# Optimization experiments

Measured on AMD Instinct MI355X. Metric: run time of the kernel, lower is better.

The kernel has to match this reference:

```python
import jax, jax.numpy as jnp
import numpy as np

QMIN, QMAX = -128, 127  # int8 range


def _quantize(x, scale, zero_point):
    """Affine quantize float -> int8: clamp(round(x/scale) + zp, -128, 127)."""
    q = jnp.round(x / scale) + zero_point
    return jnp.clip(q, QMIN, QMAX).astype(jnp.int8)


def setup_inputs() -> dict:
    key = jax.random.key(0)
    k1, k2, k3 = jax.random.split(key, 3)
    N, IN, OUT = 8192, 4096, 4096
    inp = jax.random.normal(k1, (N, IN), dtype=jnp.float32)
    # int8 weight table [OUT, IN]
    weight = jax.random.randint(k2, (OUT, IN), QMIN, QMAX + 1, dtype=jnp.int32).astype(jnp.int8)
    # int32 bias [OUT]
    bias = jax.random.randint(k3, (OUT,), -(2 ** 15), 2 ** 15, dtype=jnp.int32)
    return {
        "input": inp,
        "weight": weight,
        "bias": bias,
        "input_scale": 0.02,
        "input_zero_point": 0,
        "output_scale": 4096.0,
        "output_zero_point": 0,
    }


def reference(input, weight, bias, input_scale, input_zero_point, output_scale, output_zero_point):
    # 1) affine quantize input to int8
    q_input = _quantize(input, input_scale, input_zero_point)
    # 2) int32 matmul: F.linear(q_input.int32, weight.int32, bias.int32)
    acc = jnp.matmul(q_input.astype(jnp.int32), weight.astype(jnp.int32).T) + bias  # [N, OUT] int32
    # 3) requantize int32 accumulator to int8 with output scale/zero-point
    q_output = _quantize(acc.astype(jnp.float32), output_scale, output_zero_point)
    return q_output
```

## Files before the change

kernel.cpp:

```cpp
#include <hip/hip_runtime.h>
#include <stdint.h>

typedef int v4i __attribute__((ext_vector_type(4)));
typedef int v16i __attribute__((ext_vector_type(16)));

__device__ __forceinline__ int clamp_i8(int v) {
    return v < -128 ? -128 : (v > 127 ? 127 : v);
}

__device__ __forceinline__ void async_load16(const void* g, void* l) {
    __builtin_amdgcn_global_load_lds(
        (const __attribute__((address_space(1))) void*)g,
        (__attribute__((address_space(3))) void*)l, 16, 0, 0);
}

__global__ void quant_input_kernel(const float4* __restrict__ x, int* __restrict__ q,
                                   const float* __restrict__ scale_p,
                                   const int* __restrict__ zp_p, int n4) {
    const float inv = 1.0f / *scale_p;
    const int zp = *zp_p;
    const int stride = gridDim.x * blockDim.x;
    for (int t = blockIdx.x * blockDim.x + threadIdx.x; t < n4; t += stride) {
        float4 v = x[t];
        int q0 = clamp_i8((int)rintf(v.x * inv) + zp);
        int q1 = clamp_i8((int)rintf(v.y * inv) + zp);
        int q2 = clamp_i8((int)rintf(v.z * inv) + zp);
        int q3 = clamp_i8((int)rintf(v.w * inv) + zp);
        q[t] = (q0 & 255) | ((q1 & 255) << 8) | ((q2 & 255) << 16) | ((q3 & 255) << 24);
    }
}

__global__ void pack_weight_kernel(const int4* __restrict__ w, int* __restrict__ q, int n4) {
    const int stride = gridDim.x * blockDim.x;
    for (int t = blockIdx.x * blockDim.x + threadIdx.x; t < n4; t += stride) {
        int4 v = w[t];
        q[t] = (v.x & 255) | ((v.y & 255) << 8) | ((v.z & 255) << 16) | ((v.w & 255) << 24);
    }
}

#define BM 256
#define BN 128
#define BK 64

__global__ __launch_bounds__(256, 2) void gemm_i8_kernel(
    const int8_t* __restrict__ A, const int8_t* __restrict__ W,
    const int* __restrict__ bias, int* __restrict__ C,
    const float* __restrict__ oscale_p, const int* __restrict__ ozp_p,
    int N, int K, int M) {
    __shared__ int8_t lA[2][BM * BK];
    __shared__ int8_t lB[2][BN * BK];

    const int tid = threadIdx.x;
    const int lane = tid & 63;
    const int w = tid >> 6;
    const int wm = w >> 1;
    const int wn = w & 1;

    const int bm = blockIdx.y * BM;
    const int bn = blockIdx.x * BN;

    const int s_sub = lane >> 2;
    const int s_col = (((lane & 3) ^ ((s_sub >> 1) & 3))) * 16;
    const int8_t* gA = A + (int64_t)(bm + w * 64 + s_sub) * K + s_col;
    const int8_t* gB = W + (int64_t)(bn + w * 32 + s_sub) * K + s_col;
    const int64_t rs = (int64_t)16 * K;
    int8_t* lA0 = &lA[0][w * 4096];
    int8_t* lA1 = &lA[1][w * 4096];
    int8_t* lB0 = &lB[0][w * 2048];
    int8_t* lB1 = &lB[1][w * 2048];

    const int m0 = lane & 31;
    const int rsw = (m0 >> 1) & 3;
    const int chi = lane >> 5;

    v16i acc[4][2];
#pragma unroll
    for (int i = 0; i < 4; i++)
#pragma unroll
        for (int j = 0; j < 2; j++)
#pragma unroll
            for (int r = 0; r < 16; r++) acc[i][j][r] = 0;

    {
        async_load16(gA, lA0);
        async_load16(gA + rs, lA0 + 1024);
        async_load16(gA + 2 * rs, lA0 + 2048);
        async_load16(gA + 3 * rs, lA0 + 3072);
        async_load16(gB, lB0);
        async_load16(gB + rs, lB0 + 1024);
        gA += BK;
        gB += BK;
    }

    int cur = 0;
    for (int kt = 0; kt < K; kt += BK) {
        __syncthreads();
        if (kt + BK < K) {
            int8_t* dA = cur ? lA0 : lA1;
            int8_t* dB = cur ? lB0 : lB1;
            async_load16(gA, dA);
            async_load16(gA + rs, dA + 1024);
            async_load16(gA + 2 * rs, dA + 2048);
            async_load16(gA + 3 * rs, dA + 3072);
            async_load16(gB, dB);
            async_load16(gB + rs, dB + 1024);
            gA += BK;
            gB += BK;
        }
        const int8_t* cA = &lA[cur][0];
        const int8_t* cB = &lB[cur][0];
#pragma unroll
        for (int k0 = 0; k0 < BK; k0 += 32) {
            const int cb = k0 >> 4;
            v4i af[4], bf[2];
#pragma unroll
            for (int ms = 0; ms < 4; ms++)
                af[ms] = *(const v4i*)&cA[(wm * 128 + ms * 32 + m0) * BK +
                                          (((cb + chi) ^ rsw) << 4)];
#pragma unroll
            for (int ns = 0; ns < 2; ns++)
                bf[ns] = *(const v4i*)&cB[(wn * 64 + ns * 32 + m0) * BK +
                                          (((cb + chi) ^ rsw) << 4)];

#pragma unroll
            for (int ms = 0; ms < 4; ms++)
#pragma unroll
                for (int ns = 0; ns < 2; ns++)
                    acc[ms][ns] = __builtin_amdgcn_mfma_i32_32x32x32_i8(
                        af[ms], bf[ns], acc[ms][ns], 0, 0, 0);
        }
        cur ^= 1;
    }

    const float inv_os = 1.0f / *oscale_p;
    const int ozp = *ozp_p;
    const int rbase = 4 * (lane >> 5);
#pragma unroll
    for (int ns = 0; ns < 2; ns++) {
        const int gn = bn + wn * 64 + ns * 32 + m0;
        const int bv = bias[gn];
#pragma unroll
        for (int ms = 0; ms < 4; ms++) {
            const int gm0 = bm + wm * 128 + ms * 32 + rbase;
            v16i a = acc[ms][ns];
#pragma unroll
            for (int reg = 0; reg < 16; reg++) {
                const int row = (reg & 3) + 8 * (reg >> 2);
                int v = a[reg] + bv;
                int q = (int)rintf((float)v * inv_os) + ozp;
                q = clamp_i8(q);
                C[(int64_t)(gm0 + row) * M + gn] = q;
            }
        }
    }
}

extern "C" void kernel_launch(void* const* d_in, const int* in_sizes, int n_in,
                              void* d_out, int out_size, void* d_ws, size_t ws_size,
                              hipStream_t stream) {
    const float* x = (const float*)d_in[0];
    const int* wgt = (const int*)d_in[1];
    const int* bias = (const int*)d_in[2];
    const float* in_scale = (const float*)d_in[3];
    const int* in_zp = (const int*)d_in[4];
    const float* out_scale = (const float*)d_in[5];
    const int* out_zp = (const int*)d_in[6];

    const int64_t x_elems = (int64_t)in_sizes[0];
    const int OUT = in_sizes[2];
    const int K = in_sizes[1] / OUT;
    const int N = (int)(x_elems / K);

    int8_t* qA = (int8_t*)d_ws;
    int8_t* qW = qA + x_elems;

    {
        int n4 = (int)(x_elems / 4);
        quant_input_kernel<<<4096, 256, 0, stream>>>(
            (const float4*)x, (int*)qA, in_scale, in_zp, n4);
    }
    {
        int n4 = (int)(((int64_t)OUT * K) / 4);
        pack_weight_kernel<<<2048, 256, 0, stream>>>(
            (const int4*)wgt, (int*)qW, n4);
    }
    dim3 grid(OUT / BN, N / BM);
    gemm_i8_kernel<<<grid, 256, 0, stream>>>(qA, qW, bias, (int*)d_out,
                                             out_scale, out_zp, N, K, OUT);
}
```

Before: 419.7 us.

## Triple-buffer LDS tiles with explicit waitcnt pipeline and MFMA priority boost

Replaces the double-buffered K loop with a three-stage LDS ring. Two tiles stay in flight, and a manual vmcnt(6) wait waits only on the oldest group of async loads rather than draining the whole queue. It also raises wave priority around the MFMA block to favour matrix issue. LDS use grows from 48KB to 72KB per block, which may cut occupancy below the two blocks requested by launch bounds.

```diff
diff --git a/kernel.cpp b/kernel.cpp
--- a/kernel.cpp
+++ b/kernel.cpp
@@ -47,8 +47,8 @@
     const int* __restrict__ bias, int* __restrict__ C,
     const float* __restrict__ oscale_p, const int* __restrict__ ozp_p,
     int N, int K, int M) {
-    __shared__ int8_t lA[2][BM * BK];
-    __shared__ int8_t lB[2][BN * BK];
+    __shared__ int8_t lA[3][BM * BK];
+    __shared__ int8_t lB[3][BN * BK];
 
     const int tid = threadIdx.x;
     const int lane = tid & 63;
@@ -64,10 +64,6 @@
     const int8_t* gA = A + (int64_t)(bm + w * 64 + s_sub) * K + s_col;
     const int8_t* gB = W + (int64_t)(bn + w * 32 + s_sub) * K + s_col;
     const int64_t rs = (int64_t)16 * K;
-    int8_t* lA0 = &lA[0][w * 4096];
-    int8_t* lA1 = &lA[1][w * 4096];
-    int8_t* lB0 = &lB[0][w * 2048];
-    int8_t* lB1 = &lB[1][w * 2048];
 
     const int m0 = lane & 31;
     const int rsw = (m0 >> 1) & 3;
@@ -81,34 +77,22 @@
 #pragma unroll
             for (int r = 0; r < 16; r++) acc[i][j][r] = 0;
 
-    {
-        async_load16(gA, lA0);
-        async_load16(gA + rs, lA0 + 1024);
-        async_load16(gA + 2 * rs, lA0 + 2048);
-        async_load16(gA + 3 * rs, lA0 + 3072);
-        async_load16(gB, lB0);
-        async_load16(gB + rs, lB0 + 1024);
+    auto stage = [&](int b) {
+        int8_t* dA = &lA[b][w * 4096];
+        int8_t* dB = &lB[b][w * 2048];
+        async_load16(gA, dA);
+        async_load16(gA + rs, dA + 1024);
+        async_load16(gA + 2 * rs, dA + 2048);
+        async_load16(gA + 3 * rs, dA + 3072);
+        async_load16(gB, dB);
+        async_load16(gB + rs, dB + 1024);
         gA += BK;
         gB += BK;
-    }
+    };
 
-    int cur = 0;
-    for (int kt = 0; kt < K; kt += BK) {
-        __syncthreads();
-        if (kt + BK < K) {
-            int8_t* dA = cur ? lA0 : lA1;
-            int8_t* dB = cur ? lB0 : lB1;
-            async_load16(gA, dA);
-            async_load16(gA + rs, dA + 1024);
-            async_load16(gA + 2 * rs, dA + 2048);
-            async_load16(gA + 3 * rs, dA + 3072);
-            async_load16(gB, dB);
-            async_load16(gB + rs, dB + 1024);
-            gA += BK;
-            gB += BK;
-        }
-        const int8_t* cA = &lA[cur][0];
-        const int8_t* cB = &lB[cur][0];
+    auto compute = [&](int b) {
+        const int8_t* cA = &lA[b][0];
+        const int8_t* cB = &lB[b][0];
 #pragma unroll
         for (int k0 = 0; k0 < BK; k0 += 32) {
             const int cb = k0 >> 4;
@@ -122,15 +106,39 @@
                 bf[ns] = *(const v4i*)&cB[(wn * 64 + ns * 32 + m0) * BK +
                                           (((cb + chi) ^ rsw) << 4)];
 
+            __builtin_amdgcn_s_setprio(1);
 #pragma unroll
             for (int ms = 0; ms < 4; ms++)
 #pragma unroll
                 for (int ns = 0; ns < 2; ns++)
                     acc[ms][ns] = __builtin_amdgcn_mfma_i32_32x32x32_i8(
                         af[ms], bf[ns], acc[ms][ns], 0, 0, 0);
+            __builtin_amdgcn_s_setprio(0);
         }
-        cur ^= 1;
+    };
+
+    const int NT = K / BK;
+
+    stage(0);
+    stage(1);
+
+    int cbuf = 0;
+    int sbuf = 2;
+    for (int t = 0; t < NT - 2; ++t) {
+        asm volatile("s_waitcnt vmcnt(6) lgkmcnt(0)" ::: "memory");
+        __builtin_amdgcn_s_barrier();
+        stage(sbuf);
+        sbuf = (sbuf == 2) ? 0 : sbuf + 1;
+        compute(cbuf);
+        cbuf = (cbuf == 2) ? 0 : cbuf + 1;
     }
+    asm volatile("s_waitcnt vmcnt(6) lgkmcnt(0)" ::: "memory");
+    __builtin_amdgcn_s_barrier();
+    compute(cbuf);
+    cbuf = (cbuf == 2) ? 0 : cbuf + 1;
+    asm volatile("s_waitcnt vmcnt(0) lgkmcnt(0)" ::: "memory");
+    __builtin_amdgcn_s_barrier();
+    compute(cbuf);
 
     const float inv_os = 1.0f / *oscale_p;
     const int ozp = *ozp_p;
```

New measurement: 431.4 us. +2.8%, slower.

## Use 256x256 tiles with 8 waves and a barrier-phased ping-pong pipeline

Applied to the files above, without the earlier changes.

Each block now computes a 256x256 output tile with 512 threads (8 waves), which doubles operand reuse per block. Shared memory is arranged as two ping-pong buffers, each holding two 64-wide K sub-stages (128 K per iteration). Each iteration runs in four phases; every phase issues part of the next tile's async global-to-LDS loads, and explicit s_barrier, s_waitcnt vmcnt/lgkmcnt and s_setprio calls interleave memory traffic with MFMA work. The costs are 128KB of LDS and one block per CU, which leaves less latency hiding across blocks, plus more barriers per iteration.

```diff
diff --git a/kernel.cpp b/kernel.cpp
--- a/kernel.cpp
+++ b/kernel.cpp
@@ -39,35 +39,31 @@
 }
 
 #define BM 256
-#define BN 128
+#define BN 256
 #define BK 64
 
-__global__ __launch_bounds__(256, 2) void gemm_i8_kernel(
+__global__ __launch_bounds__(512, 1) void gemm_i8_kernel(
     const int8_t* __restrict__ A, const int8_t* __restrict__ W,
     const int* __restrict__ bias, int* __restrict__ C,
     const float* __restrict__ oscale_p, const int* __restrict__ ozp_p,
     int N, int K, int M) {
-    __shared__ int8_t lA[2][BM * BK];
-    __shared__ int8_t lB[2][BN * BK];
+    __shared__ int8_t lA[2][2][BM * BK];
+    __shared__ int8_t lB[2][2][BN * BK];
 
     const int tid = threadIdx.x;
     const int lane = tid & 63;
     const int w = tid >> 6;
-    const int wm = w >> 1;
-    const int wn = w & 1;
+    const int wm = w >> 2;
+    const int wn = w & 3;
 
     const int bm = blockIdx.y * BM;
     const int bn = blockIdx.x * BN;
 
     const int s_sub = lane >> 2;
-    const int s_col = (((lane & 3) ^ ((s_sub >> 1) & 3))) * 16;
-    const int8_t* gA = A + (int64_t)(bm + w * 64 + s_sub) * K + s_col;
-    const int8_t* gB = W + (int64_t)(bn + w * 32 + s_sub) * K + s_col;
-    const int64_t rs = (int64_t)16 * K;
-    int8_t* lA0 = &lA[0][w * 4096];
-    int8_t* lA1 = &lA[1][w * 4096];
-    int8_t* lB0 = &lB[0][w * 2048];
-    int8_t* lB1 = &lB[1][w * 2048];
+    const int s_col = ((lane & 3) ^ ((s_sub >> 1) & 3)) * 16;
+    const int8_t* gA = A + (int64_t)(bm + w * 16 + s_sub) * K + s_col;
+    const int8_t* gB = W + (int64_t)(bn + w * 16 + s_sub) * K + s_col;
+    const int64_t hstep = (int64_t)128 * K;
 
     const int m0 = lane & 31;
     const int rsw = (m0 >> 1) & 3;
@@ -81,56 +77,94 @@
 #pragma unroll
             for (int r = 0; r < 16; r++) acc[i][j][r] = 0;
 
-    {
-        async_load16(gA, lA0);
-        async_load16(gA + rs, lA0 + 1024);
-        async_load16(gA + 2 * rs, lA0 + 2048);
-        async_load16(gA + 3 * rs, lA0 + 3072);
-        async_load16(gB, lB0);
-        async_load16(gB + rs, lB0 + 1024);
-        gA += BK;
-        gB += BK;
-    }
-
-    int cur = 0;
-    for (int kt = 0; kt < K; kt += BK) {
-        __syncthreads();
-        if (kt + BK < K) {
-            int8_t* dA = cur ? lA0 : lA1;
-            int8_t* dB = cur ? lB0 : lB1;
-            async_load16(gA, dA);
-            async_load16(gA + rs, dA + 1024);
-            async_load16(gA + 2 * rs, dA + 2048);
-            async_load16(gA + 3 * rs, dA + 3072);
-            async_load16(gB, dB);
-            async_load16(gB + rs, dB + 1024);
-            gA += BK;
-            gB += BK;
+#define STAGE_A(p, s, koff)                                     \
+    do {                                                        \
+        async_load16(gA + (koff), &lA[p][s][w * 1024]);         \
+        async_load16(gA + hstep + (koff), &lA[p][s][8192 + w * 1024]); \
+    } while (0)
+#define STAGE_B(p, s, koff)                                     \
+    do {                                                        \
+        async_load16(gB + (koff), &lB[p][s][w * 1024]);         \
+        async_load16(gB + hstep + (koff), &lB[p][s][8192 + w * 1024]); \
+    } while (0)
+#define VMC4 asm volatile("s_waitcnt vmcnt(4)" ::: "memory")
+#define VMC0 asm volatile("s_waitcnt vmcnt(0)" ::: "memory")
+#define VNOP do {} while (0)
+
+#define PHASE(p, s, k0, SG, VM)                                               \
+    do {                                                                      \
+        const int8_t* cA_ = lA[p][s];                                         \
+        const int8_t* cB_ = lB[p][s];                                         \
+        const int cc_ = (((((k0) >> 4) + chi)) ^ rsw) << 4;                   \
+        v4i af_[4], bf_[2];                                                   \
+        _Pragma("unroll") for (int ms = 0; ms < 4; ms++)                      \
+            af_[ms] = *(const v4i*)&cA_[(wm * 128 + ms * 32 + m0) * BK + cc_];\
+        _Pragma("unroll") for (int ns = 0; ns < 2; ns++)                      \
+            bf_[ns] = *(const v4i*)&cB_[(wn * 64 + ns * 32 + m0) * BK + cc_]; \
+        SG;                                                                   \
+        __builtin_amdgcn_s_barrier();                                         \
+        asm volatile("s_waitcnt lgkmcnt(0)" ::: "memory");                    \
+        __builtin_amdgcn_s_setprio(1);                                        \
+        _Pragma("unroll") for (int ms = 0; ms < 4; ms++)                      \
+            _Pragma("unroll") for (int ns = 0; ns < 2; ns++)                  \
+                acc[ms][ns] = __builtin_amdgcn_mfma_i32_32x32x32_i8(          \
+                    af_[ms], bf_[ns], acc[ms][ns], 0, 0, 0);                  \
+        __builtin_amdgcn_s_setprio(0);                                        \
+        VM;                                                                   \
+        __builtin_amdgcn_s_barrier();                                         \
+    } while (0)
+
+#define ITER(cur, oth)                                     \
+    do {                                                   \
+        PHASE(cur, 0, 0,  STAGE_A(oth, 0, 0),  VNOP);      \
+        PHASE(cur, 0, 32, STAGE_B(oth, 0, 0),  VMC4);      \
+        PHASE(cur, 1, 0,  STAGE_A(oth, 1, 64), VNOP);      \
+        PHASE(cur, 1, 32, STAGE_B(oth, 1, 64), VMC4);      \
+        gA += 128;                                         \
+        gB += 128;                                         \
+    } while (0)
+
+#define LASTI(cur)                           \
+    do {                                     \
+        PHASE(cur, 0, 0,  VNOP, VNOP);       \
+        PHASE(cur, 0, 32, VNOP, VMC0);       \
+        PHASE(cur, 1, 0,  VNOP, VNOP);       \
+        PHASE(cur, 1, 32, VNOP, VNOP);       \
+    } while (0)
+
+    STAGE_A(0, 0, 0);
+    STAGE_B(0, 0, 0);
+    STAGE_A(0, 1, 64);
+    STAGE_B(0, 1, 64);
+    gA += 128;
+    gB += 128;
+    VMC4;
+    __builtin_amdgcn_s_barrier();
+
+    const int nPairs = (K / 128) - 1;
+    if (nPairs & 1) {
+        for (int i = 0; i < nPairs / 2; ++i) {
+            ITER(0, 1);
+            ITER(1, 0);
         }
-        const int8_t* cA = &lA[cur][0];
-        const int8_t* cB = &lB[cur][0];
-#pragma unroll
-        for (int k0 = 0; k0 < BK; k0 += 32) {
-            const int cb = k0 >> 4;
-            v4i af[4], bf[2];
-#pragma unroll
-            for (int ms = 0; ms < 4; ms++)
-                af[ms] = *(const v4i*)&cA[(wm * 128 + ms * 32 + m0) * BK +
-                                          (((cb + chi) ^ rsw) << 4)];
-#pragma unroll
-            for (int ns = 0; ns < 2; ns++)
-                bf[ns] = *(const v4i*)&cB[(wn * 64 + ns * 32 + m0) * BK +
-                                          (((cb + chi) ^ rsw) << 4)];
-
-#pragma unroll
-            for (int ms = 0; ms < 4; ms++)
-#pragma unroll
-                for (int ns = 0; ns < 2; ns++)
-                    acc[ms][ns] = __builtin_amdgcn_mfma_i32_32x32x32_i8(
-                        af[ms], bf[ns], acc[ms][ns], 0, 0, 0);
+        ITER(0, 1);
+        LASTI(1);
+    } else {
+        for (int i = 0; i < nPairs / 2; ++i) {
+            ITER(0, 1);
+            ITER(1, 0);
         }
-        cur ^= 1;
-    }
+        LASTI(0);
+    }
+
+#undef ITER
+#undef LASTI
+#undef PHASE
+#undef STAGE_A
+#undef STAGE_B
+#undef VMC4
+#undef VMC0
+#undef VNOP
 
     const float inv_os = 1.0f / *oscale_p;
     const int ozp = *ozp_p;
@@ -185,6 +219,6 @@
             (const int4*)wgt, (int*)qW, n4);
     }
     dim3 grid(OUT / BN, N / BM);
-    gemm_i8_kernel<<<grid, 256, 0, stream>>>(qA, qW, bias, (int*)d_out,
+    gemm_i8_kernel<<<grid, 512, 0, stream>>>(qA, qW, bias, (int*)d_out,
                                              out_scale, out_zp, N, K, OUT);
 }
```

Measured after the change: 426.6 us. No clear change (+1.7%).

## Prepack weights into MFMA fragment order and load B directly to registers

Applied to the files above, without the earlier changes.

The weight pack kernel now writes int8 weights in per-lane MFMA fragment order, so each wave can load its B operands straight from global memory into registers with coalesced 16-byte loads. The B tile is no longer staged in LDS, which cuts LDS traffic and footprint. B fragments for the next K step are loaded after the current MFMAs, giving a register-level prefetch. In exchange, B reads are no longer shared through LDS across the two wm waves, so global and L2 reads of B double. Load latency is now hidden only by the MFMA work of a single iteration.

```diff
diff --git a/kernel.cpp b/kernel.cpp
--- a/kernel.cpp
+++ b/kernel.cpp
@@ -30,11 +30,26 @@
     }
 }
 
-__global__ void pack_weight_kernel(const int4* __restrict__ w, int* __restrict__ q, int n4) {
+__global__ void pack_weight_kernel(const int* __restrict__ w, int4* __restrict__ q,
+                                   int K, int nfrag) {
     const int stride = gridDim.x * blockDim.x;
-    for (int t = blockIdx.x * blockDim.x + threadIdx.x; t < n4; t += stride) {
-        int4 v = w[t];
-        q[t] = (v.x & 255) | ((v.y & 255) << 8) | ((v.z & 255) << 16) | ((v.w & 255) << 24);
+    const int Kc32 = K / 32;
+    for (int t = blockIdx.x * blockDim.x + threadIdx.x; t < nfrag; t += stride) {
+        const int l = t & 63;
+        const int rest = t >> 6;
+        const int k32 = rest % Kc32;
+        const int c32 = rest / Kc32;
+        const int col = c32 * 32 + (l & 31);
+        const int kb = k32 * 32 + (l >> 5) * 16;
+        const int* src = w + (int64_t)col * K + kb;
+        int4 out;
+        int* op = (int*)&out;
+#pragma unroll
+        for (int j = 0; j < 4; j++) {
+            int4 v = *(const int4*)(src + 4 * j);
+            op[j] = (v.x & 255) | ((v.y & 255) << 8) | ((v.z & 255) << 16) | ((v.w & 255) << 24);
+        }
+        q[t] = out;
     }
 }
 
@@ -48,7 +63,6 @@
     const float* __restrict__ oscale_p, const int* __restrict__ ozp_p,
     int N, int K, int M) {
     __shared__ int8_t lA[2][BM * BK];
-    __shared__ int8_t lB[2][BN * BK];
 
     const int tid = threadIdx.x;
     const int lane = tid & 63;
@@ -62,12 +76,14 @@
     const int s_sub = lane >> 2;
     const int s_col = (((lane & 3) ^ ((s_sub >> 1) & 3))) * 16;
     const int8_t* gA = A + (int64_t)(bm + w * 64 + s_sub) * K + s_col;
-    const int8_t* gB = W + (int64_t)(bn + w * 32 + s_sub) * K + s_col;
     const int64_t rs = (int64_t)16 * K;
     int8_t* lA0 = &lA[0][w * 4096];
     int8_t* lA1 = &lA[1][w * 4096];
-    int8_t* lB0 = &lB[0][w * 2048];
-    int8_t* lB1 = &lB[1][w * 2048];
+
+    const int Kc32 = K >> 5;
+    const int8_t* pB = W + ((int64_t)(blockIdx.x * (BN / 32) + wn * 2) * Kc32 * 64 +
+                            lane) * 16;
+    const int64_t nsoff = (int64_t)Kc32 * 1024;
 
     const int m0 = lane & 31;
     const int rsw = (m0 >> 1) & 3;
@@ -80,54 +96,56 @@
         for (int j = 0; j < 2; j++)
 #pragma unroll
             for (int r = 0; r < 16; r++) acc[i][j][r] = 0;
+
+    v4i bf[2][2];
 
     {
         async_load16(gA, lA0);
         async_load16(gA + rs, lA0 + 1024);
         async_load16(gA + 2 * rs, lA0 + 2048);
         async_load16(gA + 3 * rs, lA0 + 3072);
-        async_load16(gB, lB0);
-        async_load16(gB + rs, lB0 + 1024);
         gA += BK;
-        gB += BK;
+        bf[0][0] = *(const v4i*)(pB);
+        bf[1][0] = *(const v4i*)(pB + 1024);
+        bf[0][1] = *(const v4i*)(pB + nsoff);
+        bf[1][1] = *(const v4i*)(pB + nsoff + 1024);
+        pB += 2048;
     }
 
     int cur = 0;
     for (int kt = 0; kt < K; kt += BK) {
         __syncthreads();
-        if (kt + BK < K) {
+        const bool more = (kt + BK < K);
+        if (more) {
             int8_t* dA = cur ? lA0 : lA1;
-            int8_t* dB = cur ? lB0 : lB1;
             async_load16(gA, dA);
             async_load16(gA + rs, dA + 1024);
             async_load16(gA + 2 * rs, dA + 2048);
             async_load16(gA + 3 * rs, dA + 3072);
-            async_load16(gB, dB);
-            async_load16(gB + rs, dB + 1024);
             gA += BK;
-            gB += BK;
         }
         const int8_t* cA = &lA[cur][0];
-        const int8_t* cB = &lB[cur][0];
 #pragma unroll
         for (int k0 = 0; k0 < BK; k0 += 32) {
             const int cb = k0 >> 4;
-            v4i af[4], bf[2];
+            v4i af[4];
 #pragma unroll
             for (int ms = 0; ms < 4; ms++)
                 af[ms] = *(const v4i*)&cA[(wm * 128 + ms * 32 + m0) * BK +
                                           (((cb + chi) ^ rsw) << 4)];
 #pragma unroll
-            for (int ns = 0; ns < 2; ns++)
-                bf[ns] = *(const v4i*)&cB[(wn * 64 + ns * 32 + m0) * BK +
-                                          (((cb + chi) ^ rsw) << 4)];
-
-#pragma unroll
             for (int ms = 0; ms < 4; ms++)
 #pragma unroll
                 for (int ns = 0; ns < 2; ns++)
                     acc[ms][ns] = __builtin_amdgcn_mfma_i32_32x32x32_i8(
-                        af[ms], bf[ns], acc[ms][ns], 0, 0, 0);
+                        af[ms], bf[k0 >> 5][ns], acc[ms][ns], 0, 0, 0);
+        }
+        if (more) {
+            bf[0][0] = *(const v4i*)(pB);
+            bf[1][0] = *(const v4i*)(pB + 1024);
+            bf[0][1] = *(const v4i*)(pB + nsoff);
+            bf[1][1] = *(const v4i*)(pB + nsoff + 1024);
+            pB += 2048;
         }
         cur ^= 1;
     }
@@ -180,9 +198,9 @@
             (const float4*)x, (int*)qA, in_scale, in_zp, n4);
     }
     {
-        int n4 = (int)(((int64_t)OUT * K) / 4);
+        int nfrag = (int)(((int64_t)OUT * K) / 16);
         pack_weight_kernel<<<2048, 256, 0, stream>>>(
-            (const int4*)wgt, (int*)qW, n4);
+            (const int*)wgt, (int4*)qW, K, nfrag);
     }
     dim3 grid(OUT / BN, N / BM);
     gemm_i8_kernel<<<grid, 256, 0, stream>>>(qA, qW, bias, (int*)d_out,
```

Result: no change. 425.1 us (+1.3%).
